# Kernel tuning notes

Measured on AMD Instinct MI355X. Metric: run time of the kernel, lower is better.

## Reference

```python
import jax, jax.numpy as jnp
import numpy as np
from jax import lax

CAP_N = 3
ROUTE_NUM = 3


def squash(s, axis=-1):
    # v = (|s|^2 / (1+|s|^2)) * s / |s|
    n2 = jnp.sum(s * s, axis=axis, keepdims=True)
    return (n2 / (1.0 + n2)) * s * lax.rsqrt(n2 + 1e-8)


def cap_layer2(x, W, bias, b0, num_out_caps, out_dim, as_final):
    # x: [bs, in_dim, H, W]; W: [out_dim*num_out_caps, in_dim] (1x1 conv)
    bs = x.shape[0]
    pred = jnp.einsum('oc,bchw->bohw', W, x) + bias[None, :, None, None]
    pred = pred.reshape(bs, num_out_caps, out_dim, -1)      # [bs, out_caps, d, in_caps]
    pred = jnp.transpose(pred, (0, 3, 1, 2))                # [bs, in_caps, out_caps, d]
    b = b0                                                   # [bs, out_caps, in_caps]
    v = None
    for _ in range(ROUTE_NUM):
        c = jax.nn.softmax(b, axis=1)                        # softmax over out_caps
        s = jnp.einsum('boi,biod->bod', c, pred)             # [bs, out_caps, d]
        v = squash(s)
        db = lax.stop_gradient(jnp.einsum('bod,biod->boi', v, pred))
        b = b + db
    if not as_final:
        side = int(np.sqrt(num_out_caps))
        v = jnp.transpose(v, (0, 2, 1)).reshape(bs, out_dim, side, side)
    return v


def setup_inputs() -> dict:
    key = jax.random.key(0)
    ks = jax.random.split(key, 8)
    bs = 128
    x = jax.random.normal(ks[0], (bs, 64, 8, 8), dtype=jnp.float32)
    Wb = jax.random.normal(ks[1], (64, 64, 3, 3), dtype=jnp.float32) * 0.05
    bb = jnp.zeros((64,), dtype=jnp.float32)
    W1 = jax.random.normal(ks[2], (4096, 64), dtype=jnp.float32) * 0.05
    b1 = jnp.zeros((4096,), dtype=jnp.float32)
    W2 = jax.random.normal(ks[3], (640, 64), dtype=jnp.float32) * 0.05
    b2 = jnp.zeros((640,), dtype=jnp.float32)
    b_basic = jax.random.uniform(ks[4], (CAP_N, bs, 64, 64), dtype=jnp.float32)
    b_cls = jax.random.uniform(ks[5], (bs, 10, 64), dtype=jnp.float32)
    return {'x': x, 'Wb': Wb, 'bb': bb, 'W1': W1, 'b1': b1, 'W2': W2, 'b2': b2,
            'b_basic': b_basic, 'b_cls': b_cls}


def reference(x, Wb, bb, W1, b1, W2, b2, b_basic, b_cls):
    # buffer: 3x3 conv + ReLU
    h = lax.conv_general_dilated(x, Wb, (1, 1), 'SAME',
                                 dimension_numbers=('NCHW', 'OIHW', 'NCHW'))
    h = jax.nn.relu(h + bb[None, :, None, None])
    # _do_squash over channel dim per spatial location
    h = squash(h, axis=1)
    for i in range(CAP_N):
        h = cap_layer2(h, W1, b1, b_basic[i], 64, 64, False)
    v = cap_layer2(h, W2, b2, b_cls, 10, 64, True)   # [bs, 10, 64]
    return v
```

## Files before the change

kernel.cpp:

```cpp
#include <hip/hip_runtime.h>
#include <math.h>
#include <type_traits>


#define SYS_ST(p, v) __hip_atomic_store((p), (v), __ATOMIC_RELAXED, __HIP_MEMORY_SCOPE_SYSTEM)
#define SYS_LD(p)    __hip_atomic_load((p), __ATOMIC_RELAXED, __HIP_MEMORY_SCOPE_SYSTEM)

typedef float v4f __attribute__((ext_vector_type(4)));

__device__ __forceinline__ void sys_st4(float* p, float4 q) {
    v4f v; v[0] = q.x; v[1] = q.y; v[2] = q.z; v[3] = q.w;
    asm volatile("global_store_dwordx4 %0, %1, off sc0 sc1" :: "v"(p), "v"(v) : "memory");
}

__global__ __launch_bounds__(256) void prep_kernel(
    const float* __restrict__ x, const float* __restrict__ Wb,
    const float* __restrict__ bb,
    const float* __restrict__ W1, const float* __restrict__ b1,
    const float* __restrict__ W2, const float* __restrict__ b2,
    float* __restrict__ h,
    float* __restrict__ WT1, float* __restrict__ G1,
    float* __restrict__ gb1, float* __restrict__ bb21,
    float* __restrict__ WT2, float* __restrict__ G2,
    float* __restrict__ gb2, float* __restrict__ bb22,
    int* __restrict__ flags)
{
    __shared__ float smem[10560];
    const int blk = blockIdx.x;
    const int t = threadIdx.x;

    if (blk < 128) {
        float* xs  = smem;
        float* hs  = smem + 6400;
        float* scl = smem + 10496;
        const int b = blk;
        for (int idx = t; idx < 6400; idx += 256) xs[idx] = 0.f;
        __syncthreads();
        #pragma unroll
        for (int k = 0; k < 4; ++k) {
            int idx4 = t + k * 256;
            float4 v = *(const float4*)&x[(size_t)b * 4096 + idx4 * 4];
            int e0 = idx4 * 4;
            int c  = e0 >> 6;
            int hw = e0 & 63;
            int r = hw >> 3, cc = hw & 7;
            float* xp = &xs[c * 100 + (r + 1) * 10 + (cc + 1)];
            xp[0] = v.x; xp[1] = v.y; xp[2] = v.z; xp[3] = v.w;
        }
        __syncthreads();
        const int oc = t >> 2;
        const int hg = t & 3;
        float acc[16];
        #pragma unroll
        for (int k = 0; k < 16; ++k) acc[k] = 0.f;
        const float* wp = Wb + (size_t)oc * 64 * 9;
        for (int ic = 0; ic < 64; ++ic) {
            float w[9];
            #pragma unroll
            for (int j = 0; j < 9; ++j) w[j] = wp[ic * 9 + j];
            const float* xr = &xs[ic * 100];
            #pragma unroll
            for (int k = 0; k < 16; ++k) {
                int hw = hg * 16 + k;
                int r = hw >> 3, cc = hw & 7;
                int p0 = r * 10 + cc;
                float a = acc[k];
                a = fmaf(w[0], xr[p0],      a);
                a = fmaf(w[1], xr[p0 + 1],  a);
                a = fmaf(w[2], xr[p0 + 2],  a);
                a = fmaf(w[3], xr[p0 + 10], a);
                a = fmaf(w[4], xr[p0 + 11], a);
                a = fmaf(w[5], xr[p0 + 12], a);
                a = fmaf(w[6], xr[p0 + 20], a);
                a = fmaf(w[7], xr[p0 + 21], a);
                a = fmaf(w[8], xr[p0 + 22], a);
                acc[k] = a;
            }
        }
        float bias = bb[oc];
        #pragma unroll
        for (int k = 0; k < 16; ++k) {
            float v = acc[k] + bias;
            v = v > 0.f ? v : 0.f;
            hs[oc * 64 + hg * 16 + k] = v;
        }
        __syncthreads();
        if (t < 64) {
            float n2 = 0.f;
            for (int c = 0; c < 64; ++c) { float v = hs[c * 64 + t]; n2 = fmaf(v, v, n2); }
            scl[t] = (n2 / (1.f + n2)) * rsqrtf(n2 + 1e-8f);
        }
        __syncthreads();
        #pragma unroll
        for (int k = 0; k < 4; ++k) {
            int idx4 = t + k * 256;
            int e0 = idx4 * 4;
            int hw0 = e0 & 63;
            float4 o;
            o.x = hs[e0 + 0] * scl[hw0 + 0];
            o.y = hs[e0 + 1] * scl[hw0 + 1];
            o.z = hs[e0 + 2] * scl[hw0 + 2];
            o.w = hs[e0 + 3] * scl[hw0 + 3];
            *(float4*)&h[(size_t)b * 4096 + e0] = o;
        }
    } else if (blk < 202) {
        const bool w1 = blk < 192;
        const int o = w1 ? (blk - 128) : (blk - 192);
        const float* W    = w1 ? W1 : W2;
        const float* bias = w1 ? b1 : b2;
        float* WT  = w1 ? WT1  : WT2;
        float* G   = w1 ? G1   : G2;
        float* gb  = w1 ? gb1  : gb2;
        float* bb2 = w1 ? bb21 : bb22;
        float* WS = smem;
        #pragma unroll
        for (int p = 0; p < 4; ++p) {
            int idx = t + p * 256;
            int d = idx >> 4, c0 = (idx & 15) * 4;
            *(float4*)&WS[d * 68 + c0] =
                *(const float4*)&W[((size_t)o * 64 + d) * 64 + c0];
        }
        __syncthreads();
        const int Q = t & 15, R = t >> 4;
        #pragma unroll
        for (int p = 0; p < 4; ++p) {
            int c = R + 16 * p;
            float4 v;
            v.x = WS[(4 * Q + 0) * 68 + c];
            v.y = WS[(4 * Q + 1) * 68 + c];
            v.z = WS[(4 * Q + 2) * 68 + c];
            v.w = WS[(4 * Q + 3) * 68 + c];
            *(float4*)&WT[((size_t)o * 64 + c) * 64 + 4 * Q] = v;
        }
        const int c1 = t >> 2, j = t & 3;
        float acc[16];
        #pragma unroll
        for (int g = 0; g < 16; ++g) acc[g] = 0.f;
        for (int d = 0; d < 64; ++d) {
            float a = WS[d * 68 + c1];
            #pragma unroll
            for (int g = 0; g < 16; ++g)
                acc[g] = fmaf(a, WS[d * 68 + j * 16 + g], acc[g]);
        }
        #pragma unroll
        for (int g = 0; g < 16; ++g)
            G[(size_t)o * 4096 + c1 * 64 + j * 16 + g] = acc[g];
        if (t < 64) {
            float s = 0.f;
            for (int d = 0; d < 64; ++d) s = fmaf(bias[o * 64 + d], WS[d * 68 + t], s);
            gb[o * 64 + t] = s;
        }
        if (t == 0) {
            float s = 0.f;
            for (int d = 0; d < 64; ++d) { float bv = bias[o * 64 + d]; s = fmaf(bv, bv, s); }
            bb2[o] = s;
        }
    } else if (blk == 202) {
        for (int i = t; i < 4096; i += 256) flags[i] = 0;
    }
}

__global__ __launch_bounds__(1024, 4) void caps_fused(
    const float* __restrict__ h0,
    const float* __restrict__ WT1, const float* __restrict__ G1,
    const float* __restrict__ gb1, const float* __restrict__ bb21,
    const float* __restrict__ b1,
    const float* __restrict__ WT2, const float* __restrict__ G2,
    const float* __restrict__ gb2, const float* __restrict__ bb22,
    const float* __restrict__ b2,
    const float* __restrict__ b_basic, const float* __restrict__ b_cls,
    float* __restrict__ xbuf,
    float* __restrict__ vbuf,
    int*   __restrict__ flags,
    float* __restrict__ out)
{
    __shared__ float HC[8704];
    __shared__ float CC[2048];
    __shared__ float PP[10240];

    const int B    = blockIdx.x;
    const int q    = B >> 6;
    const int p    = B & 63;
    const int t    = threadIdx.x;
    const int wv   = t >> 6;
    const int lane = t & 63;
    const int Q    = lane & 15;
    const int GG   = lane >> 4;
    int step = 1, dcnt = 0;

    #pragma unroll
    for (int s = 0; s < 2; ++s) {
        float4 v = *(const float4*)&h0[(size_t)(2 * p + s) * 4096 + t * 4];
        int c = t >> 4, i0 = (t & 15) * 4;
        *(float4*)&HC[s * 4352 + c * 68 + i0] = v;
    }

    auto layer = [&](auto finc, const float* __restrict__ WT,
                     const float* __restrict__ Gm,
                     const float* __restrict__ gbp,
                     const float* __restrict__ bb2p,
                     const float* __restrict__ biasp,
                     const float* __restrict__ bsrc) {
        constexpr bool FIN = decltype(finc)::value;
        const int o   = FIN ? wv : q * 16 + wv;
        const bool act = !FIN || wv < 10;
        const int row0 = (wv * 2) * 64, row1 = (wv * 2 + 1) * 64;

        float bl0 = 0.f, bl1 = 0.f, gbl = 0.f, bb2o = 0.f;
        float4 gbv4 = make_float4(0.f, 0.f, 0.f, 0.f);
        float4 bias4 = gbv4;
        const float* pG  = Gm;
        const float* pWT = WT;
        if (act) {
            pG  = Gm + o * 4096 + GG * 64 + 4 * Q;
            pWT = WT + o * 4096 + GG * 64 + 4 * Q;
            gbl  = gbp[o * 64 + lane];
            gbv4 = *(const float4*)&gbp[o * 64 + 4 * Q];
            bb2o = bb2p[o];
            bias4 = *(const float4*)&biasp[o * 64 + 4 * Q];
            if (FIN) {
                bl0 = b_cls[(size_t)(2 * p) * 640 + o * 64 + lane];
                bl1 = b_cls[(size_t)(2 * p + 1) * 640 + o * 64 + lane];
            } else {
                bl0 = bsrc[o * 64 + lane];
                bl1 = bsrc[4096 + o * 64 + lane];
            }
        }

        for (int it = 0; it < 3; ++it) {
            float cc0 = 0.f, cc1 = 0.f;
            if (act) { cc0 = expf(bl0); cc1 = expf(bl1); }
            PP[wv * 64 + lane] = cc0;
            PP[1024 + wv * 64 + lane] = cc1;
            __syncthreads();
            float bp0 = 0.f, bp1 = 0.f;
            #pragma unroll
            for (int w = 0; w < 16; ++w) {
                bp0 += PP[w * 64 + lane];
                bp1 += PP[1024 + w * 64 + lane];
            }
            if (!FIN) {
                float* xb = xbuf + ((size_t)(dcnt & 1) * 256 + B) * 128;
                if (wv == 0) {
                    SYS_ST(&xb[lane], bp0);
                    SYS_ST(&xb[64 + lane], bp1);
                    asm volatile("s_waitcnt vmcnt(0)" ::: "memory");
                    if (lane == 0) SYS_ST(&flags[B * 16], step);
                    if (lane < 3) {
                        int qq = lane + (lane >= q);
                        while (SYS_LD(&flags[(qq * 64 + p) * 16]) < step) {}
                    }
                }
                __syncthreads();
                #pragma unroll
                for (int j = 0; j < 3; ++j) {
                    int qq = j + (j >= q);
                    const float* xp = xbuf + ((size_t)(dcnt & 1) * 256 + qq * 64 + p) * 128;
                    bp0 += SYS_LD(&xp[lane]);
                    bp1 += SYS_LD(&xp[64 + lane]);
                }
                ++step; ++dcnt;
            }
            float sc0 = 0.f, sc1 = 0.f;
            if (act) {
                float cv0 = cc0 / bp0, cv1 = cc1 / bp1;
                CC[row0 + lane] = cv0;
                CC[row1 + lane] = cv1;
                float a0 = cv0, a1 = cv1;
                #pragma unroll
                for (int m = 1; m < 64; m <<= 1) {
                    a0 += __shfl_xor(a0, m, 64);
                    a1 += __shfl_xor(a1, m, 64);
                }
                sc0 = a0; sc1 = a1;
            }
            __builtin_amdgcn_wave_barrier();

            float y0 = 0.f, y1 = 0.f;
            if (act) {
                #pragma unroll 8
                for (int k = 0; k < 16; ++k) {
                    float4 h40 = *(const float4*)&HC[lane * 68 + 4 * k];
                    float4 c40 = *(const float4*)&CC[row0 + 4 * k];
                    y0 = fmaf(h40.x, c40.x, y0); y0 = fmaf(h40.y, c40.y, y0);
                    y0 = fmaf(h40.z, c40.z, y0); y0 = fmaf(h40.w, c40.w, y0);
                    float4 h41 = *(const float4*)&HC[4352 + lane * 68 + 4 * k];
                    float4 c41 = *(const float4*)&CC[row1 + 4 * k];
                    y1 = fmaf(h41.x, c41.x, y1); y1 = fmaf(h41.y, c41.y, y1);
                    y1 = fmaf(h41.z, c41.z, y1); y1 = fmaf(h41.w, c41.w, y1);
                }
            }
            __builtin_amdgcn_wave_barrier();
            if (act) { CC[row0 + lane] = y0; CC[row1 + lane] = y1; }
            __builtin_amdgcn_wave_barrier();

            if (it < 2) {
                float4 a0 = make_float4(0.f, 0.f, 0.f, 0.f), a1 = a0;
                if (act) {
                    #pragma unroll 8
                    for (int k = 0; k < 16; ++k) {
                        float4 w4 = *(const float4*)&pG[k << 8];
                        float yb0 = CC[row0 + 4 * k + GG];
                        float yb1 = CC[row1 + 4 * k + GG];
                        a0.x = fmaf(w4.x, yb0, a0.x); a0.y = fmaf(w4.y, yb0, a0.y);
                        a0.z = fmaf(w4.z, yb0, a0.z); a0.w = fmaf(w4.w, yb0, a0.w);
                        a1.x = fmaf(w4.x, yb1, a1.x); a1.y = fmaf(w4.y, yb1, a1.y);
                        a1.z = fmaf(w4.z, yb1, a1.z); a1.w = fmaf(w4.w, yb1, a1.w);
                    }
                    #pragma unroll
                    for (int m = 16; m <= 32; m <<= 1) {
                        a0.x += __shfl_xor(a0.x, m, 64); a0.y += __shfl_xor(a0.y, m, 64);
                        a0.z += __shfl_xor(a0.z, m, 64); a0.w += __shfl_xor(a0.w, m, 64);
                        a1.x += __shfl_xor(a1.x, m, 64); a1.y += __shfl_xor(a1.y, m, 64);
                        a1.z += __shfl_xor(a1.z, m, 64); a1.w += __shfl_xor(a1.w, m, 64);
                    }
                }
                float vd0 = 0.f, vd1 = 0.f;
                if (act) {
                    float4 y40 = *(const float4*)&CC[row0 + 4 * Q];
                    float4 y41 = *(const float4*)&CC[row1 + 4 * Q];
                    float n20 = y40.x * a0.x + y40.y * a0.y + y40.z * a0.z + y40.w * a0.w;
                    float n21 = y41.x * a1.x + y41.y * a1.y + y41.z * a1.z + y41.w * a1.w;
                    #pragma unroll
                    for (int m = 1; m <= 8; m <<= 1) {
                        n20 += __shfl_xor(n20, m, 64);
                        n21 += __shfl_xor(n21, m, 64);
                    }
                    float yg0 = y0 * gbl, yg1 = y1 * gbl;
                    #pragma unroll
                    for (int m = 1; m < 64; m <<= 1) {
                        yg0 += __shfl_xor(yg0, m, 64);
                        yg1 += __shfl_xor(yg1, m, 64);
                    }
                    n20 = n20 + 2.f * sc0 * yg0 + sc0 * sc0 * bb2o;
                    n21 = n21 + 2.f * sc1 * yg1 + sc1 * sc1 * bb2o;
                    float s0 = (n20 / (1.f + n20)) * rsqrtf(n20 + 1e-8f);
                    float s1 = (n21 / (1.f + n21)) * rsqrtf(n21 + 1e-8f);
                    vd0 = s0 * (yg0 + sc0 * bb2o);
                    vd1 = s1 * (yg1 + sc1 * bb2o);
                    if (GG == 0) {
                        float4 u0, u1;
                        u0.x = s0 * (a0.x + sc0 * gbv4.x); u0.y = s0 * (a0.y + sc0 * gbv4.y);
                        u0.z = s0 * (a0.z + sc0 * gbv4.z); u0.w = s0 * (a0.w + sc0 * gbv4.w);
                        u1.x = s1 * (a1.x + sc1 * gbv4.x); u1.y = s1 * (a1.y + sc1 * gbv4.y);
                        u1.z = s1 * (a1.z + sc1 * gbv4.z); u1.w = s1 * (a1.w + sc1 * gbv4.w);
                        *(float4*)&CC[row0 + 4 * Q] = u0;
                        *(float4*)&CC[row1 + 4 * Q] = u1;
                    }
                }
                __builtin_amdgcn_wave_barrier();

                if (act) {
                    float4 d0 = make_float4(0.f, 0.f, 0.f, 0.f), d1 = d0;
                    #pragma unroll 8
                    for (int k = 0; k < 16; ++k) {
                        int c = 4 * k + GG;
                        float4 hc0 = *(const float4*)&HC[c * 68 + 4 * Q];
                        float ub0 = CC[row0 + c];
                        d0.x = fmaf(ub0, hc0.x, d0.x); d0.y = fmaf(ub0, hc0.y, d0.y);
                        d0.z = fmaf(ub0, hc0.z, d0.z); d0.w = fmaf(ub0, hc0.w, d0.w);
                        float4 hc1 = *(const float4*)&HC[4352 + c * 68 + 4 * Q];
                        float ub1 = CC[row1 + c];
                        d1.x = fmaf(ub1, hc1.x, d1.x); d1.y = fmaf(ub1, hc1.y, d1.y);
                        d1.z = fmaf(ub1, hc1.z, d1.z); d1.w = fmaf(ub1, hc1.w, d1.w);
                    }
                    #pragma unroll
                    for (int m = 16; m <= 32; m <<= 1) {
                        d0.x += __shfl_xor(d0.x, m, 64); d0.y += __shfl_xor(d0.y, m, 64);
                        d0.z += __shfl_xor(d0.z, m, 64); d0.w += __shfl_xor(d0.w, m, 64);
                        d1.x += __shfl_xor(d1.x, m, 64); d1.y += __shfl_xor(d1.y, m, 64);
                        d1.z += __shfl_xor(d1.z, m, 64); d1.w += __shfl_xor(d1.w, m, 64);
                    }
                    if (GG == 0) {
                        *(float4*)&CC[row0 + 4 * Q] = d0;
                        *(float4*)&CC[row1 + 4 * Q] = d1;
                    }
                }
                __builtin_amdgcn_wave_barrier();
                if (act) {
                    bl0 += CC[row0 + lane] + vd0;
                    bl1 += CC[row1 + lane] + vd1;
                }
            } else {
                if (act) {
                    float4 s40 = make_float4(0.f, 0.f, 0.f, 0.f), s41 = s40;
                    #pragma unroll 8
                    for (int k = 0; k < 16; ++k) {
                        float4 w4 = *(const float4*)&pWT[k << 8];
                        float yb0 = CC[row0 + 4 * k + GG];
                        float yb1 = CC[row1 + 4 * k + GG];
                        s40.x = fmaf(w4.x, yb0, s40.x); s40.y = fmaf(w4.y, yb0, s40.y);
                        s40.z = fmaf(w4.z, yb0, s40.z); s40.w = fmaf(w4.w, yb0, s40.w);
                        s41.x = fmaf(w4.x, yb1, s41.x); s41.y = fmaf(w4.y, yb1, s41.y);
                        s41.z = fmaf(w4.z, yb1, s41.z); s41.w = fmaf(w4.w, yb1, s41.w);
                    }
                    #pragma unroll
                    for (int m = 16; m <= 32; m <<= 1) {
                        s40.x += __shfl_xor(s40.x, m, 64); s40.y += __shfl_xor(s40.y, m, 64);
                        s40.z += __shfl_xor(s40.z, m, 64); s40.w += __shfl_xor(s40.w, m, 64);
                        s41.x += __shfl_xor(s41.x, m, 64); s41.y += __shfl_xor(s41.y, m, 64);
                        s41.z += __shfl_xor(s41.z, m, 64); s41.w += __shfl_xor(s41.w, m, 64);
                    }
                    s40.x = fmaf(bias4.x, sc0, s40.x); s40.y = fmaf(bias4.y, sc0, s40.y);
                    s40.z = fmaf(bias4.z, sc0, s40.z); s40.w = fmaf(bias4.w, sc0, s40.w);
                    s41.x = fmaf(bias4.x, sc1, s41.x); s41.y = fmaf(bias4.y, sc1, s41.y);
                    s41.z = fmaf(bias4.z, sc1, s41.z); s41.w = fmaf(bias4.w, sc1, s41.w);
                    float n20 = s40.x * s40.x + s40.y * s40.y + s40.z * s40.z + s40.w * s40.w;
                    float n21 = s41.x * s41.x + s41.y * s41.y + s41.z * s41.z + s41.w * s41.w;
                    #pragma unroll
                    for (int m = 1; m <= 8; m <<= 1) {
                        n20 += __shfl_xor(n20, m, 64);
                        n21 += __shfl_xor(n21, m, 64);
                    }
                    float sl0 = (n20 / (1.f + n20)) * rsqrtf(n20 + 1e-8f);
                    float sl1 = (n21 / (1.f + n21)) * rsqrtf(n21 + 1e-8f);
                    float4 v0, v1;
                    v0.x = s40.x * sl0; v0.y = s40.y * sl0; v0.z = s40.z * sl0; v0.w = s40.w * sl0;
                    v1.x = s41.x * sl1; v1.y = s41.y * sl1; v1.z = s41.z * sl1; v1.w = s41.w * sl1;
                    if (FIN) {
                        if (q == 0 && GG == 0) {
                            *(float4*)&out[(size_t)(2 * p) * 640 + o * 64 + 4 * Q] = v0;
                            *(float4*)&out[(size_t)(2 * p + 1) * 640 + o * 64 + 4 * Q] = v1;
                        }
                    } else if (GG == 0) {
                        *(float4*)&CC[row0 + 4 * Q] = v0;
                        *(float4*)&CC[row1 + 4 * Q] = v1;
                    }
                }
            }
        }

        if (!FIN) {
            __syncthreads();
            float* vb = vbuf + (size_t)B * 2048;
            if (t < 512)
                sys_st4(&vb[t * 4], *(const float4*)&CC[t * 4]);
            asm volatile("s_waitcnt vmcnt(0)" ::: "memory");
            __syncthreads();
            if (t == 0) SYS_ST(&flags[B * 16], step);
            if (t < 3) {
                int qq = t + (t >= q);
                while (SYS_LD(&flags[(qq * 64 + p) * 16]) < step) {}
            }
            __syncthreads();
            #pragma unroll
            for (int rep = 0; rep < 2; ++rep) {
                int idx = rep * 1024 + t;
                int d = idx & 63, s = (idx >> 6) & 1, ol = idx >> 7;
                HC[s * 4352 + d * 68 + q * 16 + ol] = CC[idx];
            }
            #pragma unroll
            for (int j = 0; j < 3; ++j) {
                int qq = j + (j >= q);
                const float* vp = vbuf + (size_t)(qq * 64 + p) * 2048;
                #pragma unroll
                for (int rep = 0; rep < 2; ++rep) {
                    int idx = rep * 1024 + t;
                    int d = idx & 63, s = (idx >> 6) & 1, ol = idx >> 7;
                    HC[s * 4352 + d * 68 + qq * 16 + ol] = SYS_LD(&vp[idx]);
                }
            }
            ++step;
        }
    };

    layer(std::integral_constant<bool, false>{}, WT1, G1, gb1, bb21, b1,
          b_basic + (((size_t)0 * 128 + 2 * p) << 12));
    layer(std::integral_constant<bool, false>{}, WT1, G1, gb1, bb21, b1,
          b_basic + (((size_t)1 * 128 + 2 * p) << 12));
    layer(std::integral_constant<bool, false>{}, WT1, G1, gb1, bb21, b1,
          b_basic + (((size_t)2 * 128 + 2 * p) << 12));
    layer(std::integral_constant<bool, true>{}, WT2, G2, gb2, bb22, b2, nullptr);
}

extern "C" void kernel_launch(void* const* d_in, const int* in_sizes, int n_in,
                              void* d_out, int out_size, void* d_ws, size_t ws_size,
                              hipStream_t stream) {
    const float* x       = (const float*)d_in[0];
    const float* Wb      = (const float*)d_in[1];
    const float* bb      = (const float*)d_in[2];
    const float* W1      = (const float*)d_in[3];
    const float* b1      = (const float*)d_in[4];
    const float* W2      = (const float*)d_in[5];
    const float* b2      = (const float*)d_in[6];
    const float* b_basic = (const float*)d_in[7];
    const float* b_cls   = (const float*)d_in[8];
    float* out = (float*)d_out;

    float* h0    = (float*)d_ws;
    float* WT1   = h0   + 524288;
    float* WT2   = WT1  + 262144;
    float* G1    = WT2  + 40960;
    float* G2    = G1   + 262144;
    float* gb1   = G2   + 40960;
    float* gb2   = gb1  + 4096;
    float* bb21  = gb2  + 640;
    float* bb22  = bb21 + 64;
    float* xbuf  = bb22 + 16;
    float* vbuf  = xbuf + 65536;
    int*   flags = (int*)(vbuf + 524288);

    prep_kernel<<<203, 256, 0, stream>>>(x, Wb, bb, W1, b1, W2, b2, h0,
                                         WT1, G1, gb1, bb21,
                                         WT2, G2, gb2, bb22, flags);
    caps_fused<<<256, 1024, 0, stream>>>(h0, WT1, G1, gb1, bb21, b1,
                                         WT2, G2, gb2, bb22, b2,
                                         b_basic, b_cls, xbuf, vbuf, flags, out);
}
```

Before: 155.7 us.

## Precompute first-iteration softmax denominators and defer cross-block wait to next layer

The prep kernel now runs with 1024 threads and adds blocks that precompute, for each basic layer, the sum of exp(b0) over output capsules, so the first routing iteration skips its cross-block reduction and barrier exchange. The end-of-layer wait on peer v-buffers moves to the start of the next layer, letting the flag poll overlap with loading that layer's parameters. The yg bias dot product now uses a float4 per lane with a 16-lane shuffle reduction instead of a 64-lane one. Together these cut grid-wide synchronisation points, at the cost of extra workspace and more prep-kernel work.

```diff
diff --git a/kernel.cpp b/kernel.cpp
--- a/kernel.cpp
+++ b/kernel.cpp
@@ -13,17 +13,18 @@
     asm volatile("global_store_dwordx4 %0, %1, off sc0 sc1" :: "v"(p), "v"(v) : "memory");
 }
 
-__global__ __launch_bounds__(256) void prep_kernel(
+__global__ __launch_bounds__(1024) void prep_kernel(
     const float* __restrict__ x, const float* __restrict__ Wb,
     const float* __restrict__ bb,
     const float* __restrict__ W1, const float* __restrict__ b1,
     const float* __restrict__ W2, const float* __restrict__ b2,
+    const float* __restrict__ b_basic,
     float* __restrict__ h,
     float* __restrict__ WT1, float* __restrict__ G1,
     float* __restrict__ gb1, float* __restrict__ bb21,
     float* __restrict__ WT2, float* __restrict__ G2,
     float* __restrict__ gb2, float* __restrict__ bb22,
-    int* __restrict__ flags)
+    float* __restrict__ den0, int* __restrict__ flags)
 {
     __shared__ float smem[10560];
     const int blk = blockIdx.x;
@@ -34,34 +35,29 @@
         float* hs  = smem + 6400;
         float* scl = smem + 10496;
         const int b = blk;
-        for (int idx = t; idx < 6400; idx += 256) xs[idx] = 0.f;
+        for (int idx = t; idx < 6400; idx += 1024) xs[idx] = 0.f;
         __syncthreads();
-        #pragma unroll
-        for (int k = 0; k < 4; ++k) {
-            int idx4 = t + k * 256;
-            float4 v = *(const float4*)&x[(size_t)b * 4096 + idx4 * 4];
-            int e0 = idx4 * 4;
-            int c  = e0 >> 6;
-            int hw = e0 & 63;
+        {
+            float4 v = *(const float4*)&x[(size_t)b * 4096 + t * 4];
+            int c  = t >> 4;
+            int hw = (t & 15) * 4;
             int r = hw >> 3, cc = hw & 7;
             float* xp = &xs[c * 100 + (r + 1) * 10 + (cc + 1)];
             xp[0] = v.x; xp[1] = v.y; xp[2] = v.z; xp[3] = v.w;
         }
         __syncthreads();
-        const int oc = t >> 2;
-        const int hg = t & 3;
-        float acc[16];
-        #pragma unroll
-        for (int k = 0; k < 16; ++k) acc[k] = 0.f;
-        const float* wp = Wb + (size_t)oc * 64 * 9;
+        const int oc = t >> 4;
+        const int hg = t & 15;
+        float acc[4] = {0.f, 0.f, 0.f, 0.f};
+        const float* wp = Wb + (size_t)oc * 576;
         for (int ic = 0; ic < 64; ++ic) {
             float w[9];
             #pragma unroll
             for (int j = 0; j < 9; ++j) w[j] = wp[ic * 9 + j];
             const float* xr = &xs[ic * 100];
             #pragma unroll
-            for (int k = 0; k < 16; ++k) {
-                int hw = hg * 16 + k;
+            for (int k = 0; k < 4; ++k) {
+                int hw = hg * 4 + k;
                 int r = hw >> 3, cc = hw & 7;
                 int p0 = r * 10 + cc;
                 float a = acc[k];
@@ -79,10 +75,9 @@
         }
         float bias = bb[oc];
         #pragma unroll
-        for (int k = 0; k < 16; ++k) {
+        for (int k = 0; k < 4; ++k) {
             float v = acc[k] + bias;
-            v = v > 0.f ? v : 0.f;
-            hs[oc * 64 + hg * 16 + k] = v;
+            hs[oc * 64 + hg * 4 + k] = v > 0.f ? v : 0.f;
         }
         __syncthreads();
         if (t < 64) {
@@ -91,10 +86,8 @@
             scl[t] = (n2 / (1.f + n2)) * rsqrtf(n2 + 1e-8f);
         }
         __syncthreads();
-        #pragma unroll
-        for (int k = 0; k < 4; ++k) {
-            int idx4 = t + k * 256;
-            int e0 = idx4 * 4;
+        {
+            int e0 = t * 4;
             int hw0 = e0 & 63;
             float4 o;
             o.x = hs[e0 + 0] * scl[hw0 + 0];
@@ -113,38 +106,35 @@
         float* gb  = w1 ? gb1  : gb2;
         float* bb2 = w1 ? bb21 : bb22;
         float* WS = smem;
-        #pragma unroll
-        for (int p = 0; p < 4; ++p) {
-            int idx = t + p * 256;
-            int d = idx >> 4, c0 = (idx & 15) * 4;
+        {
+            int d = t >> 4, c0 = (t & 15) * 4;
             *(float4*)&WS[d * 68 + c0] =
                 *(const float4*)&W[((size_t)o * 64 + d) * 64 + c0];
         }
         __syncthreads();
-        const int Q = t & 15, R = t >> 4;
-        #pragma unroll
-        for (int p = 0; p < 4; ++p) {
-            int c = R + 16 * p;
+        {
+            int c = t >> 4, dq = t & 15;
             float4 v;
-            v.x = WS[(4 * Q + 0) * 68 + c];
-            v.y = WS[(4 * Q + 1) * 68 + c];
-            v.z = WS[(4 * Q + 2) * 68 + c];
-            v.w = WS[(4 * Q + 3) * 68 + c];
-            *(float4*)&WT[((size_t)o * 64 + c) * 64 + 4 * Q] = v;
-        }
-        const int c1 = t >> 2, j = t & 3;
-        float acc[16];
-        #pragma unroll
-        for (int g = 0; g < 16; ++g) acc[g] = 0.f;
-        for (int d = 0; d < 64; ++d) {
-            float a = WS[d * 68 + c1];
-            #pragma unroll
-            for (int g = 0; g < 16; ++g)
-                acc[g] = fmaf(a, WS[d * 68 + j * 16 + g], acc[g]);
-        }
-        #pragma unroll
-        for (int g = 0; g < 16; ++g)
-            G[(size_t)o * 4096 + c1 * 64 + j * 16 + g] = acc[g];
+            v.x = WS[(4 * dq + 0) * 68 + c];
+            v.y = WS[(4 * dq + 1) * 68 + c];
+            v.z = WS[(4 * dq + 2) * 68 + c];
+            v.w = WS[(4 * dq + 3) * 68 + c];
+            *(float4*)&WT[((size_t)o * 64 + c) * 64 + 4 * dq] = v;
+        }
+        {
+            int c1 = t >> 4, j = t & 15;
+            float a0 = 0.f, a1 = 0.f, a2 = 0.f, a3 = 0.f;
+            for (int d = 0; d < 64; ++d) {
+                float a = WS[d * 68 + c1];
+                const float* g4 = &WS[d * 68 + 4 * j];
+                a0 = fmaf(a, g4[0], a0);
+                a1 = fmaf(a, g4[1], a1);
+                a2 = fmaf(a, g4[2], a2);
+                a3 = fmaf(a, g4[3], a3);
+            }
+            float4 v; v.x = a0; v.y = a1; v.z = a2; v.w = a3;
+            *(float4*)&G[(size_t)o * 4096 + c1 * 64 + 4 * j] = v;
+        }
         if (t < 64) {
             float s = 0.f;
             for (int d = 0; d < 64; ++d) s = fmaf(bias[o * 64 + d], WS[d * 68 + t], s);
@@ -155,8 +145,16 @@
             for (int d = 0; d < 64; ++d) { float bv = bias[o * 64 + d]; s = fmaf(bv, bv, s); }
             bb2[o] = s;
         }
-    } else if (blk == 202) {
-        for (int i = t; i < 4096; i += 256) flags[i] = 0;
+    } else if (blk < 226) {
+        const int id = blk - 202;
+        const int L = id >> 3, grp = id & 7;
+        const int b = grp * 16 + (t >> 6), i = t & 63;
+        const float* bp = b_basic + (((size_t)L * 128 + b) << 12) + i;
+        float s = 0.f;
+        for (int o = 0; o < 64; ++o) s += expf(bp[o * 64]);
+        den0[((size_t)L * 128 + b) * 64 + i] = s;
+    } else {
+        for (int i = t; i < 4096; i += 1024) flags[i] = 0;
     }
 }
 
@@ -169,6 +167,7 @@
     const float* __restrict__ gb2, const float* __restrict__ bb22,
     const float* __restrict__ b2,
     const float* __restrict__ b_basic, const float* __restrict__ b_cls,
+    const float* __restrict__ den0,
     float* __restrict__ xbuf,
     float* __restrict__ vbuf,
     int*   __restrict__ flags,
@@ -200,13 +199,14 @@
                      const float* __restrict__ gbp,
                      const float* __restrict__ bb2p,
                      const float* __restrict__ biasp,
-                     const float* __restrict__ bsrc) {
+                     const float* __restrict__ bsrc,
+                     const float* __restrict__ den0p, bool entry) {
         constexpr bool FIN = decltype(finc)::value;
         const int o   = FIN ? wv : q * 16 + wv;
         const bool act = !FIN || wv < 10;
         const int row0 = (wv * 2) * 64, row1 = (wv * 2 + 1) * 64;
 
-        float bl0 = 0.f, bl1 = 0.f, gbl = 0.f, bb2o = 0.f;
+        float bl0 = 0.f, bl1 = 0.f, bb2o = 0.f;
         float4 gbv4 = make_float4(0.f, 0.f, 0.f, 0.f);
         float4 bias4 = gbv4;
         const float* pG  = Gm;
@@ -214,7 +214,6 @@
         if (act) {
             pG  = Gm + o * 4096 + GG * 64 + 4 * Q;
             pWT = WT + o * 4096 + GG * 64 + 4 * Q;
-            gbl  = gbp[o * 64 + lane];
             gbv4 = *(const float4*)&gbp[o * 64 + 4 * Q];
             bb2o = bb2p[o];
             bias4 = *(const float4*)&biasp[o * 64 + 4 * Q];
@@ -227,39 +226,66 @@
             }
         }
 
+        if (entry) {
+            if (t < 3) {
+                int qq = t + (t >= q);
+                while (SYS_LD(&flags[(qq * 64 + p) * 16]) < step) {}
+            }
+            __syncthreads();
+            #pragma unroll
+            for (int j = 0; j < 3; ++j) {
+                int qq = j + (j >= q);
+                const float* vp = vbuf + (size_t)(qq * 64 + p) * 2048;
+                #pragma unroll
+                for (int rep = 0; rep < 2; ++rep) {
+                    int idx = rep * 1024 + t;
+                    int d = idx & 63, s = (idx >> 6) & 1, ol = idx >> 7;
+                    HC[s * 4352 + d * 68 + qq * 16 + ol] = SYS_LD(&vp[idx]);
+                }
+            }
+            ++step;
+            __syncthreads();
+        } else {
+            __syncthreads();
+        }
+
         for (int it = 0; it < 3; ++it) {
-            float cc0 = 0.f, cc1 = 0.f;
+            float cc0 = 0.f, cc1 = 0.f, bp0 = 1.f, bp1 = 1.f;
             if (act) { cc0 = expf(bl0); cc1 = expf(bl1); }
-            PP[wv * 64 + lane] = cc0;
-            PP[1024 + wv * 64 + lane] = cc1;
-            __syncthreads();
-            float bp0 = 0.f, bp1 = 0.f;
-            #pragma unroll
-            for (int w = 0; w < 16; ++w) {
-                bp0 += PP[w * 64 + lane];
-                bp1 += PP[1024 + w * 64 + lane];
-            }
-            if (!FIN) {
-                float* xb = xbuf + ((size_t)(dcnt & 1) * 256 + B) * 128;
-                if (wv == 0) {
-                    SYS_ST(&xb[lane], bp0);
-                    SYS_ST(&xb[64 + lane], bp1);
-                    asm volatile("s_waitcnt vmcnt(0)" ::: "memory");
-                    if (lane == 0) SYS_ST(&flags[B * 16], step);
-                    if (lane < 3) {
-                        int qq = lane + (lane >= q);
-                        while (SYS_LD(&flags[(qq * 64 + p) * 16]) < step) {}
-                    }
-                }
+            if (it == 0 && !FIN) {
+                if (act) { bp0 = den0p[lane]; bp1 = den0p[64 + lane]; }
+            } else {
+                PP[wv * 64 + lane] = cc0;
+                PP[1024 + wv * 64 + lane] = cc1;
                 __syncthreads();
+                bp0 = 0.f; bp1 = 0.f;
                 #pragma unroll
-                for (int j = 0; j < 3; ++j) {
-                    int qq = j + (j >= q);
-                    const float* xp = xbuf + ((size_t)(dcnt & 1) * 256 + qq * 64 + p) * 128;
-                    bp0 += SYS_LD(&xp[lane]);
-                    bp1 += SYS_LD(&xp[64 + lane]);
-                }
-                ++step; ++dcnt;
+                for (int w = 0; w < 16; ++w) {
+                    bp0 += PP[w * 64 + lane];
+                    bp1 += PP[1024 + w * 64 + lane];
+                }
+                if (!FIN) {
+                    float* xb = xbuf + ((size_t)(dcnt & 1) * 256 + B) * 128;
+                    if (wv == 0) {
+                        SYS_ST(&xb[lane], bp0);
+                        SYS_ST(&xb[64 + lane], bp1);
+                        asm volatile("s_waitcnt vmcnt(0)" ::: "memory");
+                        if (lane == 0) SYS_ST(&flags[B * 16], step);
+                        if (lane < 3) {
+                            int qq = lane + (lane >= q);
+                            while (SYS_LD(&flags[(qq * 64 + p) * 16]) < step) {}
+                        }
+                    }
+                    __syncthreads();
+                    #pragma unroll
+                    for (int j = 0; j < 3; ++j) {
+                        int qq = j + (j >= q);
+                        const float* xp = xbuf + ((size_t)(dcnt & 1) * 256 + qq * 64 + p) * 128;
+                        bp0 += SYS_LD(&xp[lane]);
+                        bp1 += SYS_LD(&xp[64 + lane]);
+                    }
+                    ++step; ++dcnt;
+                }
             }
             float sc0 = 0.f, sc1 = 0.f;
             if (act) {
@@ -321,14 +347,12 @@
                     float4 y41 = *(const float4*)&CC[row1 + 4 * Q];
                     float n20 = y40.x * a0.x + y40.y * a0.y + y40.z * a0.z + y40.w * a0.w;
                     float n21 = y41.x * a1.x + y41.y * a1.y + y41.z * a1.z + y41.w * a1.w;
+                    float yg0 = y40.x * gbv4.x + y40.y * gbv4.y + y40.z * gbv4.z + y40.w * gbv4.w;
+                    float yg1 = y41.x * gbv4.x + y41.y * gbv4.y + y41.z * gbv4.z + y41.w * gbv4.w;
                     #pragma unroll
                     for (int m = 1; m <= 8; m <<= 1) {
                         n20 += __shfl_xor(n20, m, 64);
                         n21 += __shfl_xor(n21, m, 64);
-                    }
-                    float yg0 = y0 * gbl, yg1 = y1 * gbl;
-                    #pragma unroll
-                    for (int m = 1; m < 64; m <<= 1) {
                         yg0 += __shfl_xor(yg0, m, 64);
                         yg1 += __shfl_xor(yg1, m, 64);
                     }
@@ -438,39 +462,27 @@
             asm volatile("s_waitcnt vmcnt(0)" ::: "memory");
             __syncthreads();
             if (t == 0) SYS_ST(&flags[B * 16], step);
-            if (t < 3) {
-                int qq = t + (t >= q);
-                while (SYS_LD(&flags[(qq * 64 + p) * 16]) < step) {}
-            }
-            __syncthreads();
             #pragma unroll
             for (int rep = 0; rep < 2; ++rep) {
                 int idx = rep * 1024 + t;
                 int d = idx & 63, s = (idx >> 6) & 1, ol = idx >> 7;
                 HC[s * 4352 + d * 68 + q * 16 + ol] = CC[idx];
             }
-            #pragma unroll
-            for (int j = 0; j < 3; ++j) {
-                int qq = j + (j >= q);
-                const float* vp = vbuf + (size_t)(qq * 64 + p) * 2048;
-                #pragma unroll
-                for (int rep = 0; rep < 2; ++rep) {
-                    int idx = rep * 1024 + t;
-                    int d = idx & 63, s = (idx >> 6) & 1, ol = idx >> 7;
-                    HC[s * 4352 + d * 68 + qq * 16 + ol] = SYS_LD(&vp[idx]);
-                }
-            }
-            ++step;
+            __syncthreads();
         }
     };
 
     layer(std::integral_constant<bool, false>{}, WT1, G1, gb1, bb21, b1,
-          b_basic + (((size_t)0 * 128 + 2 * p) << 12));
+          b_basic + (((size_t)0 * 128 + 2 * p) << 12),
+          den0 + ((size_t)0 * 128 + 2 * p) * 64, false);
     layer(std::integral_constant<bool, false>{}, WT1, G1, gb1, bb21, b1,
-          b_basic + (((size_t)1 * 128 + 2 * p) << 12));
+          b_basic + (((size_t)1 * 128 + 2 * p) << 12),
+          den0 + ((size_t)1 * 128 + 2 * p) * 64, true);
     layer(std::integral_constant<bool, false>{}, WT1, G1, gb1, bb21, b1,
-          b_basic + (((size_t)2 * 128 + 2 * p) << 12));
-    layer(std::integral_constant<bool, true>{}, WT2, G2, gb2, bb22, b2, nullptr);
+          b_basic + (((size_t)2 * 128 + 2 * p) << 12),
+          den0 + ((size_t)2 * 128 + 2 * p) * 64, true);
+    layer(std::integral_constant<bool, true>{}, WT2, G2, gb2, bb22, b2,
+          nullptr, nullptr, true);
 }
 
 extern "C" void kernel_launch(void* const* d_in, const int* in_sizes, int n_in,
@@ -496,14 +508,16 @@
     float* gb2   = gb1  + 4096;
     float* bb21  = gb2  + 640;
     float* bb22  = bb21 + 64;
-    float* xbuf  = bb22 + 16;
+    float* den0  = bb22 + 16;
+    float* xbuf  = den0 + 24576;
     float* vbuf  = xbuf + 65536;
     int*   flags = (int*)(vbuf + 524288);
 
-    prep_kernel<<<203, 256, 0, stream>>>(x, Wb, bb, W1, b1, W2, b2, h0,
-                                         WT1, G1, gb1, bb21,
-                                         WT2, G2, gb2, bb22, flags);
+    prep_kernel<<<227, 1024, 0, stream>>>(x, Wb, bb, W1, b1, W2, b2, b_basic,
+                                          h0, WT1, G1, gb1, bb21,
+                                          WT2, G2, gb2, bb22, den0, flags);
     caps_fused<<<256, 1024, 0, stream>>>(h0, WT1, G1, gb1, bb21, b1,
                                          WT2, G2, gb2, bb22, b2,
-                                         b_basic, b_cls, xbuf, vbuf, flags, out);
+                                         b_basic, b_cls, den0,
+                                         xbuf, vbuf, flags, out);
 }
```

Measured after the change: 161.2 us. 1.04x slower.
